# Performance work log

Measured on AMD Instinct MI355X. Metric: run time of the kernel, lower is better.

Reference implementation:

```python
import jax, jax.numpy as jnp
import numpy as np

T, D, NPER, K = 8192, 512, 4, 6  # minority samples, dims, synthetic-per-sample, SMOTE k


def setup_inputs() -> dict:
    key = jax.random.key(0)
    k1, k2, k3 = jax.random.split(key, 3)
    min_samples = jax.random.normal(k1, (T, D), dtype=jnp.float32)
    gaps = jax.random.uniform(k2, (T, NPER), dtype=jnp.float32)
    # populate() draws randint(0, k-2) inclusive -> values in [0, K-1) = [0, 5)
    nn_choice = jax.random.randint(k3, (T, NPER), 0, K - 1, dtype=jnp.int64)
    return {"min_samples": min_samples, "gaps": gaps, "nn_choice": nn_choice}


def reference(min_samples, gaps, nn_choice):
    # --- find_k: full pairwise euclidean distance matrix [T, T] ---
    sq = jnp.sum(min_samples * min_samples, axis=1)  # [T]
    d2 = sq[:, None] + sq[None, :] - 2.0 * (min_samples @ min_samples.T)
    dist = jnp.sqrt(jnp.maximum(d2, 0.0))  # [T, T]
    # --- k_neighbors: argsort rows, drop self (col 0), keep k-1 neighbors ---
    nn_idx = jnp.argsort(dist, axis=1)[:, 1:K]  # [T, K-1] int
    # --- populate: pick a random neighbor, interpolate with random gap ---
    neigh = jnp.take_along_axis(nn_idx, nn_choice, axis=1)  # [T, NPER]
    diff = min_samples[neigh] - min_samples[:, None, :]      # [T, NPER, D]
    syn = min_samples[:, None, :] + gaps[:, :, None] * diff  # [T, NPER, D]
    # row-major reshape matches the original's (outer i, inner N) fill order
    return syn.reshape(T * NPER, D)
```

## Files before the change

### kernel.cpp

```cpp
#include <hip/hip_runtime.h>
#include <cstdint>
#include <cstddef>

#define TN   8192
#define DD   512
#define NPER 4
#define KNN  5

typedef _Float16 f16x8 __attribute__((ext_vector_type(8)));
typedef float    f32x4 __attribute__((ext_vector_type(4)));
typedef unsigned int  u32;
typedef unsigned long long u64;

#define KSCALE (-1.1920928955078125e-07f)

__device__ __forceinline__ u32 pk32(float key, int idx) {
  u32 kb = __float_as_uint(key);
  kb ^= (((int)kb >> 31) | 0x80000000u);
  return (kb & 0xFFFFE000u) | (u32)idx;
}

__device__ __forceinline__ void swins5(u32 v, u32 t[5]) {
#pragma unroll
  for (int s = 0; s < 5; ++s) {
    u32 lo = v < t[s] ? v : t[s];
    u32 hi = v < t[s] ? t[s] : v;
    t[s] = lo; v = hi;
  }
}
__device__ __forceinline__ void swins8(u32 v, u32 t[8]) {
#pragma unroll
  for (int s = 0; s < 8; ++s) {
    u32 lo = v < t[s] ? v : t[s];
    u32 hi = v < t[s] ? t[s] : v;
    t[s] = lo; v = hi;
  }
}

__device__ __forceinline__ u64 packkey64(float key, int idx) {
  u32 kb = __float_as_uint(key);
  kb ^= (((int)kb >> 31) | 0x80000000u);
  return ((u64)kb << 32) | (u32)idx;
}
__device__ __forceinline__ void ins8_64(u64 v, u64 tv[8]) {
  if (v < tv[7]) {
    tv[7] = v;
#pragma unroll
    for (int s = 7; s > 0; --s) {
      u64 lo = tv[s] < tv[s-1] ? tv[s] : tv[s-1];
      u64 hi = tv[s] < tv[s-1] ? tv[s-1] : tv[s];
      tv[s-1] = lo; tv[s] = hi;
    }
  }
}

__global__ void rowsq_kernel(const float* __restrict__ X, float* __restrict__ rowsq) {
  const int row  = (int)blockIdx.x * 4 + ((int)threadIdx.x >> 6);
  const int lane = (int)threadIdx.x & 63;
  const float4* xr = (const float4*)(X + (size_t)row * DD);
  const float4 a = xr[lane];
  const float4 b = xr[lane + 64];
  float s = a.x*a.x + a.y*a.y + a.z*a.z + a.w*a.w
          + b.x*b.x + b.y*b.y + b.z*b.z + b.w*b.w;
#pragma unroll
  for (int off = 32; off >= 1; off >>= 1) s += __shfl_down(s, off, 64);
  if (lane == 0) rowsq[row] = s;
}

__global__ void prep_blk(const float* __restrict__ X, _Float16* __restrict__ Hb) {
  const int rb16 = (int)blockIdx.x;
  const int tid  = (int)threadIdx.x;
  const int lane = tid & 63;
  const int wv   = tid >> 6;
  const int lgrp = lane >> 4;
  const int lidx = lane & 15;
  const float* src = X + (size_t)(rb16*16 + lidx) * DD + lgrp*8;
#pragma unroll
  for (int i = 0; i < 4; ++i) {
    const int kc = wv*4 + i;
    const float4 x0 = *(const float4*)(src + kc*32);
    const float4 x1 = *(const float4*)(src + kc*32 + 4);
    float xs[8] = {x0.x, x0.y, x0.z, x0.w, x1.x, x1.y, x1.z, x1.w};
    f16x8 h;
#pragma unroll
    for (int j = 0; j < 8; ++j) h[j] = (_Float16)(xs[j] * 4096.f);
    *(f16x8*)((char*)Hb + ((size_t)rb16*16 + kc)*1024 + lane*16) = h;
  }
}

__launch_bounds__(256, 1)
__global__ void gemm_top8(const _Float16* __restrict__ Hb,
                          const float* __restrict__ rowsq, u32* __restrict__ partials) {
  __shared__ u32 mg[128 * 8];
  const int tid  = (int)threadIdx.x;
  const int lane = tid & 63;
  const int w    = tid >> 6;
  const int wr   = w >> 1, wc = w & 1;
  const int q    = ((int)blockIdx.x & 7) * 128 + ((int)blockIdx.x >> 3);
  const int cb   = q & 63;
  const int rsb  = q >> 6;
  const int jb   = cb * 128;
  const int lgrp = lane >> 4;
  const int lidx = lane & 15;

  const char* Bpb = (const char*)Hb + (size_t)(cb*8 + wc*4)*16384 + lane*16;

#define LOADF(dep, apb, ksv) do {                                               \
    _Pragma("unroll")                                                           \
    for (int t = 0; t < 4; ++t)                                                 \
      fa[dep][t] = *(const f16x8*)((apb) + t*16384 + (ksv)*1024);               \
    _Pragma("unroll")                                                           \
    for (int u = 0; u < 4; ++u)                                                 \
      fb[dep][u] = *(const f16x8*)(Bpb + u*16384 + (ksv)*1024);                 \
  } while (0)

#define MFMAS(dep) do {                                                         \
    _Pragma("unroll")                                                           \
    for (int rt = 0; rt < 4; ++rt)                                              \
      _Pragma("unroll")                                                         \
      for (int cf = 0; cf < 4; ++cf)                                            \
        acc[rt][cf] = __builtin_amdgcn_mfma_f32_16x16x32_f16(fa[dep][rt],       \
                                        fb[dep][cf], acc[rt][cf], 0, 0, 0);     \
  } while (0)

  u32 t5[4][5];
#pragma unroll
  for (int c = 0; c < 4; ++c)
#pragma unroll
    for (int s = 0; s < 5; ++s) t5[c][s] = 0xFFFFFFFFu;

  for (int tt = 0; tt < 4; ++tt) {
    const int row0 = rsb * 512 + tt * 128;
    const char* Apb = (const char*)Hb + (size_t)(rsb*32 + tt*8 + wr*4)*16384 + lane*16;

    f32x4 acc[4][4] = {};
    f16x8 fa[3][4], fb[3][4];
    LOADF(0, Apb, 0);
    LOADF(1, Apb, 1);
    LOADF(2, Apb, 2);
#pragma unroll
    for (int ks = 0; ks < 16; ++ks) {
      const int d = ks % 3;
      MFMAS(d);
      if (ks + 3 < 16) LOADF(d, Apb, ks + 3);
    }

    float4 sqr[4];
#pragma unroll
    for (int t = 0; t < 4; ++t)
      sqr[t] = *(const float4*)(rowsq + row0 + wr*64 + t*16 + lgrp*4);

#pragma unroll
    for (int cf = 0; cf < 4; ++cf) {
      const int jc = jb + wc*64 + cf*16 + lidx;
#pragma unroll
      for (int t = 0; t < 4; ++t) {
        const int rbase = row0 + wr*64 + t*16 + lgrp*4;
        const float sx[4] = {sqr[t].x, sqr[t].y, sqr[t].z, sqr[t].w};
#pragma unroll
        for (int qq = 0; qq < 4; ++qq) {
          const int r = rbase + qq;
          const float key = fmaf(acc[t][cf][qq], KSCALE, sx[qq]);
          u32 v = pk32(key, r);
          v = (r == jc) ? 0xFFFFFFFFu : v;
          swins5(v, t5[cf]);
        }
      }
    }
  }

#pragma unroll
  for (int cf = 0; cf < 4; ++cf) {
    const int jc = jb + wc*64 + cf*16 + lidx;
    u32 t8[8];
#pragma unroll
    for (int s = 0; s < 5; ++s) t8[s] = t5[cf][s];
#pragma unroll
    for (int s = 5; s < 8; ++s) t8[s] = 0xFFFFFFFFu;
    {
      u32 ov[5];
#pragma unroll
      for (int s = 0; s < 5; ++s) ov[s] = __shfl_xor(t5[cf][s], 16, 64);
#pragma unroll
      for (int s = 0; s < 5; ++s) swins8(ov[s], t8);
    }
    {
      u32 ov[8];
#pragma unroll
      for (int s = 0; s < 8; ++s) ov[s] = __shfl_xor(t8[s], 32, 64);
#pragma unroll
      for (int s = 0; s < 8; ++s) swins8(ov[s], t8);
    }
    if (wr == 1 && lane < 16) {
#pragma unroll
      for (int s = 0; s < 8; ++s) mg[(wc*64 + cf*16 + lidx)*8 + s] = t8[s];
    }
    __syncthreads();
    if (wr == 0 && lane < 16) {
      const u32* om = &mg[(wc*64 + cf*16 + lidx)*8];
#pragma unroll
      for (int s = 0; s < 8; ++s) swins8(om[s], t8);
      u32* pw = partials + ((size_t)jc * 16 + rsb) * 8;
#pragma unroll
      for (int s = 0; s < 8; ++s) pw[s] = t8[s];
    }
    __syncthreads();
  }
#undef LOADF
#undef MFMAS
}

__global__ void merge_nn8(const u32* __restrict__ parts, u32* __restrict__ cand) {
  const int j    = (int)blockIdx.x * 4 + ((int)threadIdx.x >> 6);
  const int lane = (int)threadIdx.x & 63;
  u32 tv[8];
#pragma unroll
  for (int s = 0; s < 8; ++s) tv[s] = 0xFFFFFFFFu;
  swins8(parts[(size_t)j * 128 + lane], tv);
  swins8(parts[(size_t)j * 128 + 64 + lane], tv);
#pragma unroll
  for (int d = 1; d < 64; d <<= 1) {
    u32 ov[8];
#pragma unroll
    for (int s = 0; s < 8; ++s) ov[s] = __shfl_xor(tv[s], d, 64);
#pragma unroll
    for (int s = 0; s < 8; ++s) swins8(ov[s], tv);
  }
  if (lane == 0) {
#pragma unroll
    for (int s = 0; s < 8; ++s) cand[(size_t)j*8 + s] = tv[s];
  }
}

__global__ void refine_nn(const float* __restrict__ X, const float* __restrict__ rowsq,
                          const u32* __restrict__ cand, int* __restrict__ nn) {
  const int j    = (int)blockIdx.x * 4 + ((int)threadIdx.x >> 6);
  const int lane = (int)threadIdx.x & 63;
  const float4* xj = (const float4*)(X + (size_t)j * DD);
  const float4 qa = xj[lane];
  const float4 qb = xj[lane + 64];
  u64 best[8];
#pragma unroll
  for (int s = 0; s < 8; ++s) best[s] = ~0ull;
#pragma unroll
  for (int c = 0; c < 8; ++c) {
    const int r = (int)(cand[(size_t)j*8 + c] & 8191u);
    const float4* xr_ = (const float4*)(X + (size_t)r * DD);
    const float4 a = xr_[lane];
    const float4 b = xr_[lane + 64];
    float d = a.x*qa.x + a.y*qa.y + a.z*qa.z + a.w*qa.w
            + b.x*qb.x + b.y*qb.y + b.z*qb.z + b.w*qb.w;
#pragma unroll
    for (int off = 32; off >= 1; off >>= 1) d += __shfl_xor(d, off, 64);
    const float key = fmaf(-2.f, d, rowsq[r]);
    ins8_64(packkey64(key, r), best);
  }
  if (lane == 0) {
#pragma unroll
    for (int s = 0; s < KNN; ++s) nn[j*KNN + s] = (int)(u32)best[s];
  }
}

__global__ void synth_kernel(const float* __restrict__ X, const int* __restrict__ nn,
                             const float* __restrict__ gaps, const int* __restrict__ choice,
                             float* __restrict__ out) {
  const float4* X4 = (const float4*)X;
  float4* O4 = (float4*)out;
  const int base = (int)blockIdx.x * 256 + (int)threadIdx.x;
#pragma unroll
  for (int it = 0; it < 8; ++it) {
    const int f    = base + it * (2048 * 256);
    const int orow = f >> 7;
    const int d4   = f & 127;
    const int i    = orow >> 2;
    const int ch   = choice[orow];
    const int nr   = nn[i * KNN + ch];
    const float g  = gaps[orow];
    const float4 xi = X4[(size_t)i  * 128 + d4];
    const float4 xn = X4[(size_t)nr * 128 + d4];
    float4 r;
    r.x = fmaf(g, xn.x - xi.x, xi.x);
    r.y = fmaf(g, xn.y - xi.y, xi.y);
    r.z = fmaf(g, xn.z - xi.z, xi.z);
    r.w = fmaf(g, xn.w - xi.w, xi.w);
    O4[(size_t)orow * 128 + d4] = r;
  }
}

extern "C" void kernel_launch(void* const* d_in, const int* in_sizes, int n_in,
                              void* d_out, int out_size, void* d_ws, size_t ws_size,
                              hipStream_t stream) {
  const float* X      = (const float*)d_in[0];
  const float* gaps   = (const float*)d_in[1];
  const int*   choice = (const int*)  d_in[2];
  float* out = (float*)d_out;

  _Float16* Hb    = (_Float16*)d_out;
  u32*      parts = (u32*)((char*)d_out + 8388608);
  u32*      cand  = (u32*)((char*)d_out + 12582912);

  float* rowsq = (float*)d_ws;
  int*   nn    = (int*)((char*)d_ws + TN * 4);

  rowsq_kernel<<<2048, 256, 0, stream>>>(X, rowsq);
  prep_blk    <<<512,  256, 0, stream>>>(X, Hb);
  gemm_top8   <<<1024, 256, 0, stream>>>(Hb, rowsq, parts);
  merge_nn8   <<<2048, 256, 0, stream>>>(parts, cand);
  refine_nn   <<<2048, 256, 0, stream>>>(X, rowsq, cand, nn);
  synth_kernel<<<2048, 256, 0, stream>>>(X, nn, gaps, choice, out);
}
```

Baseline: 160.3 us.

## Fuse row-norm into fp16 prep and target two waves per EU in GEMM

Drops the separate row-squared-norm kernel and computes the norms inside the fp16 conversion kernel, using LDS atomics to reduce the per-row partial sums, so one launch and one extra pass over X go away. The GEMM/top-k kernel now requests two waves per EU instead of one, and its register prefetch pipeline is cut from three stages to two to fit that budget. Higher occupancy is meant to hide latency better, at the cost of a shallower software prefetch and possible register pressure or spills.

```diff
diff --git a/kernel.cpp b/kernel.cpp
--- a/kernel.cpp
+++ b/kernel.cpp
@@ -54,27 +54,19 @@
   }
 }
 
-__global__ void rowsq_kernel(const float* __restrict__ X, float* __restrict__ rowsq) {
-  const int row  = (int)blockIdx.x * 4 + ((int)threadIdx.x >> 6);
-  const int lane = (int)threadIdx.x & 63;
-  const float4* xr = (const float4*)(X + (size_t)row * DD);
-  const float4 a = xr[lane];
-  const float4 b = xr[lane + 64];
-  float s = a.x*a.x + a.y*a.y + a.z*a.z + a.w*a.w
-          + b.x*b.x + b.y*b.y + b.z*b.z + b.w*b.w;
-#pragma unroll
-  for (int off = 32; off >= 1; off >>= 1) s += __shfl_down(s, off, 64);
-  if (lane == 0) rowsq[row] = s;
-}
-
-__global__ void prep_blk(const float* __restrict__ X, _Float16* __restrict__ Hb) {
+__global__ void prep_blk(const float* __restrict__ X, _Float16* __restrict__ Hb,
+                         float* __restrict__ rowsq) {
+  __shared__ float rs[16];
   const int rb16 = (int)blockIdx.x;
   const int tid  = (int)threadIdx.x;
   const int lane = tid & 63;
   const int wv   = tid >> 6;
   const int lgrp = lane >> 4;
   const int lidx = lane & 15;
+  if (tid < 16) rs[tid] = 0.f;
+  __syncthreads();
   const float* src = X + (size_t)(rb16*16 + lidx) * DD + lgrp*8;
+  float psum = 0.f;
 #pragma unroll
   for (int i = 0; i < 4; ++i) {
     const int kc = wv*4 + i;
@@ -83,12 +75,18 @@
     float xs[8] = {x0.x, x0.y, x0.z, x0.w, x1.x, x1.y, x1.z, x1.w};
     f16x8 h;
 #pragma unroll
-    for (int j = 0; j < 8; ++j) h[j] = (_Float16)(xs[j] * 4096.f);
+    for (int j = 0; j < 8; ++j) {
+      h[j] = (_Float16)(xs[j] * 4096.f);
+      psum = fmaf(xs[j], xs[j], psum);
+    }
     *(f16x8*)((char*)Hb + ((size_t)rb16*16 + kc)*1024 + lane*16) = h;
   }
-}
-
-__launch_bounds__(256, 1)
+  atomicAdd(&rs[lidx], psum);
+  __syncthreads();
+  if (tid < 16) rowsq[rb16*16 + tid] = rs[tid];
+}
+
+__attribute__((amdgpu_flat_work_group_size(256, 256), amdgpu_waves_per_eu(2, 2)))
 __global__ void gemm_top8(const _Float16* __restrict__ Hb,
                           const float* __restrict__ rowsq, u32* __restrict__ partials) {
   __shared__ u32 mg[128 * 8];
@@ -134,15 +132,14 @@
     const char* Apb = (const char*)Hb + (size_t)(rsb*32 + tt*8 + wr*4)*16384 + lane*16;
 
     f32x4 acc[4][4] = {};
-    f16x8 fa[3][4], fb[3][4];
+    f16x8 fa[2][4], fb[2][4];
     LOADF(0, Apb, 0);
     LOADF(1, Apb, 1);
-    LOADF(2, Apb, 2);
 #pragma unroll
     for (int ks = 0; ks < 16; ++ks) {
-      const int d = ks % 3;
+      const int d = ks & 1;
       MFMAS(d);
-      if (ks + 3 < 16) LOADF(d, Apb, ks + 3);
+      if (ks + 2 < 16) LOADF(d, Apb, ks + 2);
     }
 
     float4 sqr[4];
@@ -302,8 +299,7 @@
   float* rowsq = (float*)d_ws;
   int*   nn    = (int*)((char*)d_ws + TN * 4);
 
-  rowsq_kernel<<<2048, 256, 0, stream>>>(X, rowsq);
-  prep_blk    <<<512,  256, 0, stream>>>(X, Hb);
+  prep_blk    <<<512,  256, 0, stream>>>(X, Hb, rowsq);
   gemm_top8   <<<1024, 256, 0, stream>>>(Hb, rowsq, parts);
   merge_nn8   <<<2048, 256, 0, stream>>>(parts, cand);
   refine_nn   <<<2048, 256, 0, stream>>>(X, rowsq, cand, nn);
```

After: 282.6 us. 76.4% more time.
